# Optimization experiments

Hardware: AMD Instinct MI355X
Metric: run time of the kernel (lower is better)

## Reference

```python
import jax, jax.numpy as jnp
import numpy as np

B, T, D, H = 8, 1024, 1024, 16
DK = D // H


def setup_inputs() -> dict:
    key = jax.random.key(0)
    ks = jax.random.split(key, 12)
    inp = {
        'query': jax.random.normal(ks[0], (B, T, D), dtype=jnp.float32),
        'key': jax.random.normal(ks[1], (B, T, D), dtype=jnp.float32),
        'value': jax.random.normal(ks[2], (B, T, D), dtype=jnp.float32),
        'mask': jnp.ones((1, 1, T, T), dtype=jnp.float32),
        # Dense(d_model) params: kernel [D, D] + bias [D]
        'Wq': jax.random.normal(ks[3], (D, D), dtype=jnp.float32) * 0.02,
        'bq': jnp.zeros((D,), dtype=jnp.float32),
        'Wk': jax.random.normal(ks[4], (D, D), dtype=jnp.float32) * 0.02,
        'bk': jnp.zeros((D,), dtype=jnp.float32),
        'Wv': jax.random.normal(ks[5], (D, D), dtype=jnp.float32) * 0.02,
        'bv': jnp.zeros((D,), dtype=jnp.float32),
        'Wo': jax.random.normal(ks[6], (D, D), dtype=jnp.float32) * 0.02,
        'bo': jnp.zeros((D,), dtype=jnp.float32),
    }
    return inp


def _split_heads(x):
    # [B, T, D] -> [B, H, T, DK]
    b, t, d = x.shape
    return x.reshape(b, t, H, DK).transpose(0, 2, 1, 3)


def reference(query, key, value, mask, Wq, bq, Wk, bk, Wv, bv, Wo, bo):
    q = _split_heads(query @ Wq + bq)   # [B,H,T,DK]
    k = _split_heads(key @ Wk + bk)
    v = _split_heads(value @ Wv + bv)
    # NOTE: original code scales by rsqrt(seq_len) (tf.shape(query)[2] after
    # split_heads), NOT rsqrt(d_k). We reproduce that quirk faithfully.
    scale = jax.lax.rsqrt(jnp.float32(q.shape[2]))
    w = jnp.einsum('bhtd,bhsd->bhts', q, k) * scale  # [B,H,T,T]
    w = w * mask + (-1e9) * (1.0 - mask)
    attn = jax.nn.softmax(w, axis=-1)  # dropout is identity at inference
    x = jnp.einsum('bhts,bhsd->bhtd', attn, v)
    x = x.transpose(0, 2, 1, 3).reshape(query.shape[0], query.shape[1], D)
    return x @ Wo + bo
```

## Files before the change

### kernel.cpp

```cpp
#include <hip/hip_runtime.h>
#include <math.h>


typedef __attribute__((ext_vector_type(8))) short bf16x8;
typedef __attribute__((ext_vector_type(4))) float f32x4;

#define GCAST(p) ((const __attribute__((address_space(1))) void*)(const void*)(p))
#define LCAST(p) ((__attribute__((address_space(3))) void*)(p))

__device__ __forceinline__ short f2bf(float f) {
  union { float f; unsigned u; } c; c.f = f;
  unsigned r = c.u + 0x7fffu + ((c.u >> 16) & 1u);
  return (short)(r >> 16);
}
__device__ __forceinline__ unsigned pk_trunc(float lo, float hi) {
  return __builtin_amdgcn_perm(__float_as_uint(hi), __float_as_uint(lo), 0x07060302u);
}

__global__ __launch_bounds__(256) void cvt_pair(const float* __restrict__ s0,
                                                const float* __restrict__ s1,
                                                short* __restrict__ d0,
                                                short* __restrict__ d1) {
  const float* s = blockIdx.z ? s1 : s0;
  short* d = blockIdx.z ? d1 : d0;
  size_t i = ((size_t)blockIdx.x * 256 + threadIdx.x) * 8;
  float4 a = *(const float4*)&s[i];
  float4 b = *(const float4*)&s[i + 4];
  bf16x8 o = {f2bf(a.x), f2bf(a.y), f2bf(a.z), f2bf(a.w),
              f2bf(b.x), f2bf(b.y), f2bf(b.z), f2bf(b.w)};
  *(bf16x8*)&d[i] = o;
}

__global__ __launch_bounds__(256) void cvt_w3(const float* __restrict__ W0,
                                              const float* __restrict__ W1,
                                              const float* __restrict__ W2,
                                              short* __restrict__ D0,
                                              short* __restrict__ D1,
                                              short* __restrict__ D2) {
  const int z = blockIdx.z;
  const float* W = z == 0 ? W0 : (z == 1 ? W1 : W2);
  short* Wt = z == 0 ? D0 : (z == 1 ? D1 : D2);
  const int tid = threadIdx.x;
  const int n0 = blockIdx.x * 64, k0 = blockIdx.y * 64;
  __shared__ short tile[64][72];
#pragma unroll
  for (int i = 0; i < 4; ++i) {
    int k = (tid >> 4) + i * 16;
    int n4 = (tid & 15) * 4;
    float4 w = *(const float4*)&W[(size_t)(k0 + k) * 1024 + n0 + n4];
    tile[k][n4 + 0] = f2bf(w.x);
    tile[k][n4 + 1] = f2bf(w.y);
    tile[k][n4 + 2] = f2bf(w.z);
    tile[k][n4 + 3] = f2bf(w.w);
  }
  __syncthreads();
#pragma unroll
  for (int i = 0; i < 2; ++i) {
    int n = (tid >> 3) + i * 32;
    int k8 = (tid & 7) * 8;
    bf16x8 v;
#pragma unroll
    for (int j = 0; j < 8; ++j) v[j] = tile[k8 + j][n];
    *(bf16x8*)&Wt[(size_t)(n0 + n) * 1024 + k0 + k8] = v;
  }
}

template <int OUT>
__global__ __launch_bounds__(256) void gemm_m97(
    const short* __restrict__ Aa, const short* __restrict__ Ab,
    const short* __restrict__ Ba, const short* __restrict__ Bb,
    const float* __restrict__ ca, const float* __restrict__ cb,
    void* __restrict__ oa, void* __restrict__ ob) {
  const int z = blockIdx.z;
  const short* A = z ? Ab : Aa;
  const short* Bt = z ? Bb : Ba;
  const float* bias = z ? cb : ca;
  void* outp = z ? ob : oa;

  __shared__ __align__(16) short As[128 * 32];
  __shared__ __align__(16) short Bs[128 * 32];
  const int tid = threadIdx.x, lane = tid & 63, wave = tid >> 6;
  const int mrow = lane & 15, quad = lane >> 4;
  const int wm = (wave >> 1) * 64, wn = (wave & 1) * 64;
  const int m0 = blockIdx.x * 128, n0 = blockIdx.y * 128;
  const int l2 = lane >> 2, l4 = (lane & 3) * 8;

  f32x4 acc[4][4];
#pragma unroll
  for (int i = 0; i < 4; ++i)
#pragma unroll
    for (int j = 0; j < 4; ++j) acc[i][j] = f32x4{0.f, 0.f, 0.f, 0.f};

  float bias_r[4];
#pragma unroll
  for (int nc = 0; nc < 4; ++nc) bias_r[nc] = bias[n0 + wn + nc * 16 + mrow];

  const short* Ag = A + (size_t)m0 * 1024;
  const short* Bg = Bt + (size_t)n0 * 1024;

  for (int kt = 0; kt < 32; ++kt) {
    const int kof = kt * 32;
#pragma unroll
    for (int c = 0; c < 2; ++c) {
      const int m = wave * 2 + c;
      __builtin_amdgcn_global_load_lds(
          GCAST(Ag + (size_t)(16 * m + l2) * 1024 + kof + l4),
          LCAST(&As[m * 512 + lane * 8]), 16, 0, 0);
      __builtin_amdgcn_global_load_lds(
          GCAST(Bg + (size_t)(16 * m + l2) * 1024 + kof + l4),
          LCAST(&Bs[m * 512 + lane * 8]), 16, 0, 0);
    }
    __syncthreads();
    bf16x8 af[4], bf[4];
#pragma unroll
    for (int mr = 0; mr < 4; ++mr)
      af[mr] = *(const bf16x8*)&As[(wm + mr * 16 + mrow) * 32 + quad * 8];
#pragma unroll
    for (int nc = 0; nc < 4; ++nc)
      bf[nc] = *(const bf16x8*)&Bs[(wn + nc * 16 + mrow) * 32 + quad * 8];
#pragma unroll
    for (int mr = 0; mr < 4; ++mr)
#pragma unroll
      for (int nc = 0; nc < 4; ++nc)
        acc[mr][nc] = __builtin_amdgcn_mfma_f32_16x16x32_bf16(af[mr], bf[nc], acc[mr][nc], 0, 0, 0);
    __syncthreads();
  }
#pragma unroll
  for (int mr = 0; mr < 4; ++mr)
#pragma unroll
    for (int nc = 0; nc < 4; ++nc)
#pragma unroll
      for (int r = 0; r < 4; ++r) {
        int m = m0 + wm + mr * 16 + quad * 4 + r;
        int n = n0 + wn + nc * 16 + mrow;
        float v = acc[mr][nc][r] + bias_r[nc];
        int bi = m >> 10, t = m & 1023;
        int hh = n >> 6, dk = n & 63;
        if constexpr (OUT == 0) {
          ((short*)outp)[(((size_t)bi * 16 + hh) * 1024 + t) * 64 + dk] = f2bf(v);
        } else if constexpr (OUT == 1) {
          ((short*)outp)[(((size_t)bi * 16 + hh) * 64 + dk) * 1024 + t] = f2bf(v);
        } else {
          ((float*)outp)[(size_t)m * 1024 + n] = v;
        }
      }
}

__global__ __launch_bounds__(256, 4) void flash_attn(const short* __restrict__ Qg,
                                                     const short* __restrict__ Kg,
                                                     const short* __restrict__ Vtg,
                                                     short* __restrict__ Xg) {
  __shared__ __align__(16) short Ks[2][64][32];
  __shared__ __align__(16) short Vs[2][64][32];
  __shared__ __align__(16) short P[4][32][72];
  const int tid = threadIdx.x, lane = tid & 63, wave = tid >> 6;
  const int mrow = lane & 15, quad = lane >> 4;
  const int bh = blockIdx.x, qb = blockIdx.y;
  const int b = bh >> 4, h = bh & 15;
  const short* Q = Qg + (size_t)bh * 65536;
  const short* K = Kg + (size_t)bh * 65536;
  const short* Vt = Vtg + (size_t)bh * 65536;
  const int q0 = qb * 128 + wave * 32;
  short* Pw = &P[wave][0][0];

  bf16x8 aq[2][2];
#pragma unroll
  for (int qs = 0; qs < 2; ++qs)
#pragma unroll
    for (int ki = 0; ki < 2; ++ki)
      aq[qs][ki] = *(const bf16x8*)&Q[(size_t)(q0 + qs * 16 + mrow) * 64 + ki * 32 + quad * 8];

  f32x4 oacc[2][4];
#pragma unroll
  for (int qs = 0; qs < 2; ++qs)
#pragma unroll
    for (int nc = 0; nc < 4; ++nc) oacc[qs][nc] = f32x4{0.f, 0.f, 0.f, 0.f};
  float lsum[2] = {0.f, 0.f};

  const float C = 0.03125f * 1.44269504088896f;
  const int l2 = lane >> 2, l4 = (lane & 3) * 8;

  for (int kv = 0; kv < 16; ++kv) {
    const int kb = kv * 64;
    __syncthreads();
#pragma unroll
    for (int c = 0; c < 2; ++c) {
      const int m = wave * 2 + c;
      const int ki = m >> 2, mm = m & 3;
      __builtin_amdgcn_global_load_lds(
          GCAST(K + (size_t)(kb + 16 * mm + l2) * 64 + ki * 32 + l4),
          LCAST(&Ks[ki][16 * mm][0] + lane * 8), 16, 0, 0);
      __builtin_amdgcn_global_load_lds(
          GCAST(Vt + (size_t)(16 * mm + l2) * 1024 + kb + ki * 32 + l4),
          LCAST(&Vs[ki][16 * mm][0] + lane * 8), 16, 0, 0);
    }
    __syncthreads();

    bf16x8 kf[4][2];
#pragma unroll
    for (int ss = 0; ss < 4; ++ss)
#pragma unroll
      for (int ki = 0; ki < 2; ++ki)
        kf[ss][ki] = *(const bf16x8*)&Ks[ki][ss * 16 + mrow][quad * 8];

#pragma unroll
    for (int qs = 0; qs < 2; ++qs) {
      f32x4 sT[4];
#pragma unroll
      for (int ss = 0; ss < 4; ++ss) sT[ss] = f32x4{0.f, 0.f, 0.f, 0.f};
#pragma unroll
      for (int ss = 0; ss < 4; ++ss)
#pragma unroll
        for (int ki = 0; ki < 2; ++ki)
          sT[ss] = __builtin_amdgcn_mfma_f32_16x16x32_bf16(kf[ss][ki], aq[qs][ki], sT[ss], 0, 0, 0);
#pragma unroll
      for (int ss = 0; ss < 4; ++ss) {
        float p0 = __builtin_amdgcn_exp2f(sT[ss][0] * C);
        float p1 = __builtin_amdgcn_exp2f(sT[ss][1] * C);
        float p2 = __builtin_amdgcn_exp2f(sT[ss][2] * C);
        float p3 = __builtin_amdgcn_exp2f(sT[ss][3] * C);
        lsum[qs] += (p0 + p1) + (p2 + p3);
        uint2 pk = {pk_trunc(p0, p1), pk_trunc(p2, p3)};
        *(uint2*)&Pw[(qs * 16 + mrow) * 72 + ss * 16 + quad * 4] = pk;
      }
    }
#pragma unroll
    for (int ki2 = 0; ki2 < 2; ++ki2) {
      bf16x8 pa[2];
#pragma unroll
      for (int qs = 0; qs < 2; ++qs)
        pa[qs] = *(const bf16x8*)&Pw[(qs * 16 + mrow) * 72 + ki2 * 32 + quad * 8];
#pragma unroll
      for (int nc = 0; nc < 4; ++nc) {
        bf16x8 vf = *(const bf16x8*)&Vs[ki2][nc * 16 + mrow][quad * 8];
#pragma unroll
        for (int qs = 0; qs < 2; ++qs)
          oacc[qs][nc] = __builtin_amdgcn_mfma_f32_16x16x32_bf16(pa[qs], vf, oacc[qs][nc], 0, 0, 0);
      }
    }
  }

  float rinv[2];
#pragma unroll
  for (int qs = 0; qs < 2; ++qs) {
    float v = lsum[qs];
    v += __shfl_xor(v, 16, 64);
    v += __shfl_xor(v, 32, 64);
    rinv[qs] = 1.0f / v;
  }
#pragma unroll
  for (int qs = 0; qs < 2; ++qs)
#pragma unroll
    for (int nc = 0; nc < 4; ++nc)
#pragma unroll
      for (int r = 0; r < 4; ++r) {
        float rr = __shfl(rinv[qs], quad * 4 + r, 64);
        int t = q0 + qs * 16 + quad * 4 + r;
        int dk = nc * 16 + mrow;
        Xg[((size_t)(b * 1024 + t)) * 1024 + h * 64 + dk] = f2bf(oacc[qs][nc][r] * rr);
      }
}

extern "C" void kernel_launch(void* const* d_in, const int* in_sizes, int n_in,
                              void* d_out, int out_size, void* d_ws, size_t ws_size,
                              hipStream_t stream) {
  const float* query = (const float*)d_in[0];
  const float* key   = (const float*)d_in[1];
  const float* value = (const float*)d_in[2];
  const float* Wq = (const float*)d_in[4];
  const float* bq = (const float*)d_in[5];
  const float* Wk = (const float*)d_in[6];
  const float* bk = (const float*)d_in[7];
  const float* Wv = (const float*)d_in[8];
  const float* bv = (const float*)d_in[9];
  const float* Wo = (const float*)d_in[10];
  const float* bo = (const float*)d_in[11];
  float* out = (float*)d_out;

  const size_t MB = 1024 * 1024;
  char* ws = (char*)d_ws;
  short* q_ws  = (short*)(ws);
  short* k_ws  = (short*)(ws + 16 * MB);
  short* Wtq   = (short*)(ws + 32 * MB);
  short* Wtk   = (short*)(ws + 34 * MB);
  short* Wtv   = (short*)(ws + 36 * MB);
  short* x_ws  = (short*)(ws + 32 * MB);
  short* vt_ws = (short*)(ws + 48 * MB);
  short* WoT   = q_ws;
  short* Abf_v = (short*)d_out;
  short* Abf_q = (short*)d_out;
  short* Abf_k = (short*)((char*)d_out + 16 * MB);

  dim3 gb(256);
  cvt_w3<<<dim3(16, 16, 3), gb, 0, stream>>>(Wq, Wk, Wv, Wtq, Wtk, Wtv);
  cvt_pair<<<dim3(4096, 1, 1), gb, 0, stream>>>(value, value, Abf_v, Abf_v);
  gemm_m97<1><<<dim3(64, 8, 1), gb, 0, stream>>>(Abf_v, Abf_v, Wtv, Wtv,
                                                 bv, bv, vt_ws, vt_ws);
  cvt_pair<<<dim3(4096, 1, 2), gb, 0, stream>>>(query, key, Abf_q, Abf_k);
  gemm_m97<0><<<dim3(64, 8, 2), gb, 0, stream>>>(Abf_q, Abf_k, Wtq, Wtk,
                                                 bq, bk, q_ws, k_ws);
  flash_attn<<<dim3(128, 8), gb, 0, stream>>>(q_ws, k_ws, vt_ws, x_ws);
  cvt_w3<<<dim3(16, 16, 1), gb, 0, stream>>>(Wo, Wo, Wo, WoT, WoT, WoT);
  gemm_m97<2><<<dim3(64, 8, 1), gb, 0, stream>>>(x_ws, x_ws, WoT, WoT,
                                                 bo, bo, out, out);
}
```

Measured before the change: 315.3 us.

## Replace GEMM with 256x256 double-buffered 8-wave kernel and merge conversions

The projection GEMM moves from 128x128 tiles with K=32 steps and full syncs to 256x256 tiles with 512 threads. The new kernel uses K=64 double-buffered LDS with an XOR swizzle, staged global_load_lds prefetch interleaved with MFMA phases, s_setprio and fine-grained barriers. The input and weight bf16 conversions are fused into one launch, and the V activation buffer moves to the workspace so all three conversions can run together. The larger tiles give fewer blocks (128 per GEMM) and may underfill the 256 CUs. The kernel also needs 128KB of LDS per block and many more accumulator registers.

```diff
diff --git a/kernel.cpp b/kernel.cpp
--- a/kernel.cpp
+++ b/kernel.cpp
@@ -17,18 +17,52 @@
   return __builtin_amdgcn_perm(__float_as_uint(hi), __float_as_uint(lo), 0x07060302u);
 }
 
-__global__ __launch_bounds__(256) void cvt_pair(const float* __restrict__ s0,
-                                                const float* __restrict__ s1,
-                                                short* __restrict__ d0,
-                                                short* __restrict__ d1) {
-  const float* s = blockIdx.z ? s1 : s0;
-  short* d = blockIdx.z ? d1 : d0;
-  size_t i = ((size_t)blockIdx.x * 256 + threadIdx.x) * 8;
-  float4 a = *(const float4*)&s[i];
-  float4 b = *(const float4*)&s[i + 4];
-  bf16x8 o = {f2bf(a.x), f2bf(a.y), f2bf(a.z), f2bf(a.w),
-              f2bf(b.x), f2bf(b.y), f2bf(b.z), f2bf(b.w)};
-  *(bf16x8*)&d[i] = o;
+__global__ __launch_bounds__(256) void cvt_all(
+    const float* __restrict__ qf, const float* __restrict__ kf,
+    const float* __restrict__ vf, short* __restrict__ dq,
+    short* __restrict__ dk, short* __restrict__ dv,
+    const float* __restrict__ W0, const float* __restrict__ W1,
+    const float* __restrict__ W2, short* __restrict__ T0,
+    short* __restrict__ T1, short* __restrict__ T2) {
+  __shared__ short tile[64][72];
+  const int bx = blockIdx.x, tid = threadIdx.x;
+  if (bx < 12288) {
+    const int t = bx >> 12;
+    const float* s = t == 0 ? qf : (t == 1 ? kf : vf);
+    short* d = t == 0 ? dq : (t == 1 ? dk : dv);
+    size_t i = ((size_t)(bx & 4095) * 256 + tid) * 8;
+    float4 a = *(const float4*)&s[i];
+    float4 b = *(const float4*)&s[i + 4];
+    bf16x8 o = {f2bf(a.x), f2bf(a.y), f2bf(a.z), f2bf(a.w),
+                f2bf(b.x), f2bf(b.y), f2bf(b.z), f2bf(b.w)};
+    *(bf16x8*)&d[i] = o;
+  } else {
+    const int w = bx - 12288;
+    const int z = w >> 8, wb = w & 255;
+    const float* W = z == 0 ? W0 : (z == 1 ? W1 : W2);
+    short* Wt = z == 0 ? T0 : (z == 1 ? T1 : T2);
+    const int n0 = (wb & 15) * 64, k0 = (wb >> 4) * 64;
+#pragma unroll
+    for (int i = 0; i < 4; ++i) {
+      int k = (tid >> 4) + i * 16;
+      int n4 = (tid & 15) * 4;
+      float4 ww = *(const float4*)&W[(size_t)(k0 + k) * 1024 + n0 + n4];
+      tile[k][n4 + 0] = f2bf(ww.x);
+      tile[k][n4 + 1] = f2bf(ww.y);
+      tile[k][n4 + 2] = f2bf(ww.z);
+      tile[k][n4 + 3] = f2bf(ww.w);
+    }
+    __syncthreads();
+#pragma unroll
+    for (int i = 0; i < 2; ++i) {
+      int n = (tid >> 3) + i * 32;
+      int k8 = (tid & 7) * 8;
+      bf16x8 v;
+#pragma unroll
+      for (int j = 0; j < 8; ++j) v[j] = tile[k8 + j][n];
+      *(bf16x8*)&Wt[(size_t)(n0 + n) * 1024 + k0 + k8] = v;
+    }
+  }
 }
 
 __global__ __launch_bounds__(256) void cvt_w3(const float* __restrict__ W0,
@@ -66,7 +100,7 @@
 }
 
 template <int OUT>
-__global__ __launch_bounds__(256) void gemm_m97(
+__global__ __launch_bounds__(512, 2) void gemm8p(
     const short* __restrict__ Aa, const short* __restrict__ Ab,
     const short* __restrict__ Ba, const short* __restrict__ Bb,
     const float* __restrict__ ca, const float* __restrict__ cb,
@@ -77,73 +111,148 @@
   const float* bias = z ? cb : ca;
   void* outp = z ? ob : oa;
 
-  __shared__ __align__(16) short As[128 * 32];
-  __shared__ __align__(16) short Bs[128 * 32];
+  __shared__ __align__(16) short As[2][256][64];
+  __shared__ __align__(16) short Bs[2][256][64];
+  short* AsF = &As[0][0][0];
+  short* BsF = &Bs[0][0][0];
+
   const int tid = threadIdx.x, lane = tid & 63, wave = tid >> 6;
   const int mrow = lane & 15, quad = lane >> 4;
-  const int wm = (wave >> 1) * 64, wn = (wave & 1) * 64;
-  const int m0 = blockIdx.x * 128, n0 = blockIdx.y * 128;
-  const int l2 = lane >> 2, l4 = (lane & 3) * 8;
-
-  f32x4 acc[4][4];
-#pragma unroll
-  for (int i = 0; i < 4; ++i)
-#pragma unroll
-    for (int j = 0; j < 4; ++j) acc[i][j] = f32x4{0.f, 0.f, 0.f, 0.f};
-
-  float bias_r[4];
-#pragma unroll
-  for (int nc = 0; nc < 4; ++nc) bias_r[nc] = bias[n0 + wn + nc * 16 + mrow];
+  const int wm = wave >> 2, wn = wave & 3;
+  const int m0 = blockIdx.x * 256, n0 = blockIdx.y * 256;
+  const int ax = (mrow & 4) << 2;
+
+  const int idx0 = tid, idx1 = 512 + tid;
+  const int r0s = idx0 >> 3, r1s = idx1 >> 3;
+  const int c0s = ((idx0 & 7) * 8) ^ ((r0s & 4) << 2);
+  const int c1s = ((idx1 & 7) * 8) ^ ((r1s & 4) << 2);
 
   const short* Ag = A + (size_t)m0 * 1024;
   const short* Bg = Bt + (size_t)n0 * 1024;
 
-  for (int kt = 0; kt < 32; ++kt) {
-    const int kof = kt * 32;
-#pragma unroll
-    for (int c = 0; c < 2; ++c) {
-      const int m = wave * 2 + c;
-      __builtin_amdgcn_global_load_lds(
-          GCAST(Ag + (size_t)(16 * m + l2) * 1024 + kof + l4),
-          LCAST(&As[m * 512 + lane * 8]), 16, 0, 0);
-      __builtin_amdgcn_global_load_lds(
-          GCAST(Bg + (size_t)(16 * m + l2) * 1024 + kof + l4),
-          LCAST(&Bs[m * 512 + lane * 8]), 16, 0, 0);
-    }
-    __syncthreads();
-    bf16x8 af[4], bf[4];
-#pragma unroll
-    for (int mr = 0; mr < 4; ++mr)
-      af[mr] = *(const bf16x8*)&As[(wm + mr * 16 + mrow) * 32 + quad * 8];
-#pragma unroll
-    for (int nc = 0; nc < 4; ++nc)
-      bf[nc] = *(const bf16x8*)&Bs[(wn + nc * 16 + mrow) * 32 + quad * 8];
-#pragma unroll
-    for (int mr = 0; mr < 4; ++mr)
-#pragma unroll
-      for (int nc = 0; nc < 4; ++nc)
-        acc[mr][nc] = __builtin_amdgcn_mfma_f32_16x16x32_bf16(af[mr], bf[nc], acc[mr][nc], 0, 0, 0);
-    __syncthreads();
-  }
-#pragma unroll
-  for (int mr = 0; mr < 4; ++mr)
-#pragma unroll
-    for (int nc = 0; nc < 4; ++nc)
-#pragma unroll
-      for (int r = 0; r < 4; ++r) {
-        int m = m0 + wm + mr * 16 + quad * 4 + r;
-        int n = n0 + wn + nc * 16 + mrow;
-        float v = acc[mr][nc][r] + bias_r[nc];
-        int bi = m >> 10, t = m & 1023;
-        int hh = n >> 6, dk = n & 63;
-        if constexpr (OUT == 0) {
-          ((short*)outp)[(((size_t)bi * 16 + hh) * 1024 + t) * 64 + dk] = f2bf(v);
-        } else if constexpr (OUT == 1) {
-          ((short*)outp)[(((size_t)bi * 16 + hh) * 64 + dk) * 1024 + t] = f2bf(v);
-        } else {
-          ((float*)outp)[(size_t)m * 1024 + n] = v;
+  f32x4 acc[8][4];
+#pragma unroll
+  for (int i = 0; i < 8; ++i)
+#pragma unroll
+    for (int j = 0; j < 4; ++j) acc[i][j] = f32x4{0.f, 0.f, 0.f, 0.f};
+
+  float bias_r[4];
+#pragma unroll
+  for (int nc = 0; nc < 4; ++nc) bias_r[nc] = bias[n0 + wn * 64 + nc * 16 + mrow];
+
+#define STG(GP, LB, bd, h, kt)                                               \
+  __builtin_amdgcn_global_load_lds(                                          \
+      GCAST((GP) + (size_t)((h)*128 + r0s) * 1024 + (kt)*64 + c0s),          \
+      LCAST((LB) + (bd)*16384 + (h)*8192 + idx0 * 8), 16, 0, 0);             \
+  __builtin_amdgcn_global_load_lds(                                          \
+      GCAST((GP) + (size_t)((h)*128 + r1s) * 1024 + (kt)*64 + c1s),          \
+      LCAST((LB) + (bd)*16384 + (h)*8192 + idx1 * 8), 16, 0, 0)
+
+#define RDA(d, bd, mr, kh)                                                   \
+  d = *(const bf16x8*)(AsF + (bd)*16384 + (wm * 128 + (mr)*16 + mrow) * 64 + \
+                       (((kh)*32 + quad * 8) ^ ax))
+#define RDB(d, bd, nc, kh)                                                   \
+  d = *(const bf16x8*)(BsF + (bd)*16384 + (wn * 64 + (nc)*16 + mrow) * 64 +  \
+                       (((kh)*32 + quad * 8) ^ ax))
+
+#define MM(q, nc)                                                            \
+  acc[2*(q)][nc] = __builtin_amdgcn_mfma_f32_16x16x32_bf16(                  \
+      a00, bfr[nc][0], acc[2*(q)][nc], 0, 0, 0);                             \
+  acc[2*(q)][nc] = __builtin_amdgcn_mfma_f32_16x16x32_bf16(                  \
+      a01, bfr[nc][1], acc[2*(q)][nc], 0, 0, 0);                             \
+  acc[2*(q)+1][nc] = __builtin_amdgcn_mfma_f32_16x16x32_bf16(                \
+      a10, bfr[nc][0], acc[2*(q)+1][nc], 0, 0, 0);                           \
+  acc[2*(q)+1][nc] = __builtin_amdgcn_mfma_f32_16x16x32_bf16(                \
+      a11, bfr[nc][1], acc[2*(q)+1][nc], 0, 0, 0)
+
+#define PH(bd, q, VM)                                                        \
+  {                                                                          \
+    bf16x8 a00, a01, a10, a11;                                               \
+    RDA(a00, bd, 2 * (q), 0);                                                \
+    RDA(a01, bd, 2 * (q), 1);                                                \
+    RDA(a10, bd, 2 * (q) + 1, 0);                                            \
+    RDA(a11, bd, 2 * (q) + 1, 1);                                            \
+    if ((q) == 0) {                                                          \
+      RDB(bfr[0][0], bd, 0, 0); RDB(bfr[0][1], bd, 0, 1);                    \
+      RDB(bfr[1][0], bd, 1, 0); RDB(bfr[1][1], bd, 1, 1);                    \
+      RDB(bfr[2][0], bd, 2, 0); RDB(bfr[2][1], bd, 2, 1);                    \
+      RDB(bfr[3][0], bd, 3, 0); RDB(bfr[3][1], bd, 3, 1);                    \
+    }                                                                        \
+    asm volatile("" ::: "memory");                                           \
+    __builtin_amdgcn_s_barrier();                                            \
+    asm volatile("s_waitcnt lgkmcnt(0)" ::: "memory");                       \
+    __builtin_amdgcn_s_setprio(1);                                           \
+    MM(q, 0); MM(q, 1); MM(q, 2); MM(q, 3);                                  \
+    __builtin_amdgcn_s_setprio(0);                                           \
+    if (VM) asm volatile("s_waitcnt vmcnt(4)" ::: "memory");                 \
+    asm volatile("" ::: "memory");                                           \
+    __builtin_amdgcn_s_barrier();                                            \
+    asm volatile("" ::: "memory");                                           \
+  }
+
+  STG(Ag, AsF, 0, 0, 0);
+  STG(Ag, AsF, 0, 1, 0);
+  STG(Bg, BsF, 0, 0, 0);
+  STG(Bg, BsF, 0, 1, 0);
+  STG(Bg, BsF, 1, 0, 1);
+  STG(Bg, BsF, 1, 1, 1);
+  asm volatile("s_waitcnt vmcnt(4)" ::: "memory");
+  __builtin_amdgcn_s_barrier();
+  asm volatile("" ::: "memory");
+
+  bf16x8 bfr[4][2];
+#pragma unroll 1
+  for (int it = 0; it < 8; ++it) {
+    const int t1 = 2 * it + 1;
+    const int t2 = it < 7 ? 2 * it + 2 : 15;
+    const int t3 = it < 7 ? 2 * it + 3 : 15;
+    STG(Ag, AsF, 1, 0, t1); PH(0, 0, 0);
+    STG(Ag, AsF, 1, 1, t1); PH(0, 1, 0);
+    STG(Bg, BsF, 0, 0, t2); PH(0, 2, 0);
+    STG(Bg, BsF, 0, 1, t2); PH(0, 3, 1);
+    STG(Ag, AsF, 0, 0, t2); PH(1, 0, 0);
+    STG(Ag, AsF, 0, 1, t2); PH(1, 1, 0);
+    STG(Bg, BsF, 1, 0, t3); PH(1, 2, 0);
+    STG(Bg, BsF, 1, 1, t3); PH(1, 3, 1);
+  }
+  asm volatile("s_waitcnt vmcnt(0)" ::: "memory");
+
+#pragma unroll
+  for (int mr = 0; mr < 8; ++mr) {
+    const int mb = m0 + wm * 128 + mr * 16 + quad * 4;
+#pragma unroll
+    for (int nc = 0; nc < 4; ++nc) {
+      const int n = n0 + wn * 64 + nc * 16 + mrow;
+      if constexpr (OUT == 1) {
+        const int bi = mb >> 10, t = mb & 1023;
+        const int hh = n >> 6, dk = n & 63;
+        short4 pk;
+        pk.x = f2bf(acc[mr][nc][0] + bias_r[nc]);
+        pk.y = f2bf(acc[mr][nc][1] + bias_r[nc]);
+        pk.z = f2bf(acc[mr][nc][2] + bias_r[nc]);
+        pk.w = f2bf(acc[mr][nc][3] + bias_r[nc]);
+        *(short4*)&((short*)outp)[(((size_t)bi * 16 + hh) * 64 + dk) * 1024 + t] = pk;
+      } else {
+#pragma unroll
+        for (int r = 0; r < 4; ++r) {
+          const int m = mb + r;
+          const float v = acc[mr][nc][r] + bias_r[nc];
+          if constexpr (OUT == 0) {
+            const int bi = m >> 10, t = m & 1023;
+            const int hh = n >> 6, dk = n & 63;
+            ((short*)outp)[(((size_t)bi * 16 + hh) * 1024 + t) * 64 + dk] = f2bf(v);
+          } else {
+            ((float*)outp)[(size_t)m * 1024 + n] = v;
+          }
         }
       }
+    }
+  }
+#undef STG
+#undef RDA
+#undef RDB
+#undef MM
+#undef PH
 }
 
 __global__ __launch_bounds__(256, 4) void flash_attn(const short* __restrict__ Qg,
@@ -279,6 +388,7 @@
 
   const size_t MB = 1024 * 1024;
   char* ws = (char*)d_ws;
+  short* Abf_v = (short*)(ws);
   short* q_ws  = (short*)(ws);
   short* k_ws  = (short*)(ws + 16 * MB);
   short* Wtq   = (short*)(ws + 32 * MB);
@@ -287,20 +397,18 @@
   short* x_ws  = (short*)(ws + 32 * MB);
   short* vt_ws = (short*)(ws + 48 * MB);
   short* WoT   = q_ws;
-  short* Abf_v = (short*)d_out;
   short* Abf_q = (short*)d_out;
   short* Abf_k = (short*)((char*)d_out + 16 * MB);
 
-  dim3 gb(256);
-  cvt_w3<<<dim3(16, 16, 3), gb, 0, stream>>>(Wq, Wk, Wv, Wtq, Wtk, Wtv);
-  cvt_pair<<<dim3(4096, 1, 1), gb, 0, stream>>>(value, value, Abf_v, Abf_v);
-  gemm_m97<1><<<dim3(64, 8, 1), gb, 0, stream>>>(Abf_v, Abf_v, Wtv, Wtv,
-                                                 bv, bv, vt_ws, vt_ws);
-  cvt_pair<<<dim3(4096, 1, 2), gb, 0, stream>>>(query, key, Abf_q, Abf_k);
-  gemm_m97<0><<<dim3(64, 8, 2), gb, 0, stream>>>(Abf_q, Abf_k, Wtq, Wtk,
-                                                 bq, bk, q_ws, k_ws);
-  flash_attn<<<dim3(128, 8), gb, 0, stream>>>(q_ws, k_ws, vt_ws, x_ws);
-  cvt_w3<<<dim3(16, 16, 1), gb, 0, stream>>>(Wo, Wo, Wo, WoT, WoT, WoT);
-  gemm_m97<2><<<dim3(64, 8, 1), gb, 0, stream>>>(x_ws, x_ws, WoT, WoT,
-                                                 bo, bo, out, out);
-}
+  cvt_all<<<dim3(13056), dim3(256), 0, stream>>>(query, key, value,
+                                                 Abf_q, Abf_k, Abf_v,
+                                                 Wq, Wk, Wv, Wtq, Wtk, Wtv);
+  gemm8p<1><<<dim3(32, 4, 1), dim3(512), 0, stream>>>(Abf_v, Abf_v, Wtv, Wtv,
+                                                      bv, bv, vt_ws, vt_ws);
+  gemm8p<0><<<dim3(32, 4, 2), dim3(512), 0, stream>>>(Abf_q, Abf_k, Wtq, Wtk,
+                                                      bq, bk, q_ws, k_ws);
+  flash_attn<<<dim3(128, 8), dim3(256), 0, stream>>>(q_ws, k_ws, vt_ws, x_ws);
+  cvt_w3<<<dim3(16, 16, 1), dim3(256), 0, stream>>>(Wo, Wo, Wo, WoT, WoT, WoT);
+  gemm8p<2><<<dim3(32, 4, 1), dim3(512), 0, stream>>>(x_ws, x_ws, WoT, WoT,
+                                                      bo, bo, (void*)out, (void*)out);
+}
```

After: 327.8 us. +4.0%, slower.
